# Kernel optimization log

Hardware: AMD Instinct MI355X
Metric: run time of the kernel (lower is better)

Reference implementation:

```python
import jax, jax.numpy as jnp
import numpy as np

N_NUM = 2048      # recurrent neurons (== input_num)
E_NUM = 1638
OUT_NUM = 512     # readout size
TIME_CONST = 0.1  # LIF leak


def setup_inputs() -> dict:
    key = jax.random.key(0)
    k1, k2, k3, k4, k5 = jax.random.split(key, 5)
    B = 4096
    return {
        "i_": jax.random.normal(k1, (B, N_NUM), dtype=jnp.float32),
        "x": jax.random.normal(k2, (B, N_NUM), dtype=jnp.float32),
        "r": jax.random.normal(k3, (N_NUM, N_NUM), dtype=jnp.float32) * (1.0 / np.sqrt(N_NUM)),
        "f": jax.random.normal(k4, (N_NUM, OUT_NUM), dtype=jnp.float32) * (1.0 / np.sqrt(N_NUM)),
        "b": jax.random.normal(k5, (N_NUM,), dtype=jnp.float32) * 0.01,
    }


def reference(i_, x, r, f, b):
    # EI sign vector: ei_mask is a diagonal matrix diag(signs); mm(ei_mask, A) == signs[:, None] * A
    signs = jnp.where(jnp.arange(N_NUM) < E_NUM, 1.0, -1.0).astype(i_.dtype)
    self_mask = 1.0 - jnp.eye(N_NUM, dtype=i_.dtype)  # no_self: zero diagonal

    # LIF state update: x <- (1 - tau) * x + tau * (i_ + b)   (noise_coeff = 0)
    x_new = (1.0 - TIME_CONST) * x + TIME_CONST * (i_ + b)
    u = jax.nn.relu(x_new)

    # Dale's law + self-mask on recurrent weights; Dale on feedforward weights
    r_eff = signs[:, None] * jnp.abs(r * self_mask)   # [N, N]
    f_eff = signs[:, None] * jnp.abs(f)               # [N, OUT]

    f_out = u @ f_eff   # [B, OUT]
    r_out = u @ r_eff   # [B, N]
    return (f_out, r_out, u)
```

## Files before the change

### kernel.cpp

```cpp
#include <hip/hip_runtime.h>
#include <hip/hip_bf16.h>

#define B_NUM 4096
#define N_NUM 2048
#define E_NUM 1638
#define OUT_NUM 512
#define NTOT 2560
#define KDIM 2048
#define NKT 32

typedef unsigned short u16;
typedef __attribute__((ext_vector_type(8))) __bf16 bf16x8;
typedef __attribute__((ext_vector_type(4))) float f32x4;

__device__ __forceinline__ u16 f2bf(float f) {
  union { float f; unsigned u; } v; v.f = f;
  unsigned r = v.u + 0x7fffu + ((v.u >> 16) & 1u);
  return (u16)(r >> 16);
}

__device__ __forceinline__ void gload16(const u16* src, u16* dst) {
  __builtin_amdgcn_global_load_lds((__attribute__((address_space(1))) void*)src,
                                   (__attribute__((address_space(3))) void*)dst,
                                   16, 0, 0);
}

#define BAR() do { asm volatile("" ::: "memory"); \
                   __builtin_amdgcn_s_barrier();  \
                   asm volatile("" ::: "memory"); } while (0)

__global__ __launch_bounds__(256) void prep_u(const float* __restrict__ in_i,
                                              const float* __restrict__ in_x,
                                              const float* __restrict__ bias,
                                              float* __restrict__ u_f32,
                                              u16* __restrict__ u_bf16) {
  const int t = blockIdx.x * 256 + threadIdx.x;
  const int e = t * 4;
  const float4 iv = *(const float4*)(in_i + e);
  const float4 xv = *(const float4*)(in_x + e);
  const float4 bv = *(const float4*)(bias + (e & (N_NUM - 1)));
  float4 u;
  u.x = fmaxf(0.f, 0.9f * xv.x + 0.1f * (iv.x + bv.x));
  u.y = fmaxf(0.f, 0.9f * xv.y + 0.1f * (iv.y + bv.y));
  u.z = fmaxf(0.f, 0.9f * xv.z + 0.1f * (iv.z + bv.z));
  u.w = fmaxf(0.f, 0.9f * xv.w + 0.1f * (iv.w + bv.w));
  *(float4*)(u_f32 + e) = u;
  ushort4 ub;
  ub.x = f2bf(u.x); ub.y = f2bf(u.y); ub.z = f2bf(u.z); ub.w = f2bf(u.w);
  *(ushort4*)(u_bf16 + e) = ub;
}

__global__ __launch_bounds__(256) void prep_w(const float* __restrict__ r,
                                              const float* __restrict__ f,
                                              u16* __restrict__ wt) {
  __shared__ u16 ldsT[64][72];
  const int k0 = blockIdx.y * 64;
  const int n0 = blockIdx.x * 64;
  const int tid = threadIdx.x;
  const int rloc = tid >> 4;
  const int c4 = (tid & 15) * 4;
#pragma unroll
  for (int rr = 0; rr < 4; ++rr) {
    const int kl = rr * 16 + rloc;
    const int k = k0 + kl;
    const float sign = (k < E_NUM) ? 1.f : -1.f;
    float4 v;
    if (n0 < N_NUM) v = *(const float4*)(r + k * N_NUM + n0 + c4);
    else            v = *(const float4*)(f + k * OUT_NUM + (n0 - N_NUM) + c4);
    float vals[4] = {v.x, v.y, v.z, v.w};
#pragma unroll
    for (int j = 0; j < 4; ++j) {
      float val = sign * fabsf(vals[j]);
      if (n0 < N_NUM && (n0 + c4 + j) == k) val = 0.f;
      ldsT[c4 + j][kl] = f2bf(val);
    }
  }
  __syncthreads();
  const int nl = tid >> 2;
  const int kc = (tid & 3) * 16;
  u16* dst = wt + (n0 + nl) * KDIM + k0 + kc;
  *(uint4*)(dst) = *(const uint4*)&ldsT[nl][kc];
  *(uint4*)(dst + 8) = *(const uint4*)&ldsT[nl][kc + 8];
}

__global__ __launch_bounds__(256, 2) void gemm4(const u16* __restrict__ U,
                                                const u16* __restrict__ Wt,
                                                float* __restrict__ out) {
  __shared__ u16 lds[2][2][128 * 64];
  const int t = threadIdx.x;
  const int w = t >> 6, lane = t & 63;
  const int lr = lane & 15, lg = lane >> 4;
  const int wm = w >> 1, wn = w & 1;
  const int row0 = blockIdx.y * 128;
  const int col0 = blockIdx.x * 128;

  const int srow = t >> 3;
  const int koff = 8 * ((t & 7) ^ (srow & 7));
  const u16* aS = U  + (row0 + srow) * KDIM + koff;
  const u16* bS = Wt + (col0 + srow) * KDIM + koff;
  const int stBase = w * 512;

  const int arow = wm * 64 + lr;
  const int brow = wn * 64 + lr;
  const int xs = (lr & 7) << 4;
  const int ca0 = ((lg * 16) ^ xs) >> 1;
  const int ca1 = ((64 + lg * 16) ^ xs) >> 1;

  f32x4 acc[4][4] = {};

#define STAGE_A(c, kt) { const int k0_ = (kt) * 64;                         \
  _Pragma("unroll") for (int i_ = 0; i_ < 4; ++i_)                          \
    gload16(aS + i_ * 32 * KDIM + k0_, &lds[c][0][i_ * 2048 + stBase]); }
#define STAGE_B(c, kt) { const int k0_ = (kt) * 64;                         \
  _Pragma("unroll") for (int i_ = 0; i_ < 4; ++i_)                          \
    gload16(bS + i_ * 32 * KDIM + k0_, &lds[c][1][i_ * 2048 + stBase]); }

  STAGE_B(0, 0);
  STAGE_A(0, 0);
  STAGE_B(1, 1);
  asm volatile("s_waitcnt vmcnt(4)" ::: "memory");
  __builtin_amdgcn_sched_barrier(0);
  BAR();

  for (int T = 0; T < NKT; ++T) {
    const int c = T & 1;
    const u16* lA = lds[c][0];
    const u16* lB = lds[c][1];
    bf16x8 bf[4][2], af[2][2];
#pragma unroll
    for (int ni = 0; ni < 4; ++ni) {
      bf[ni][0] = *(const bf16x8*)&lB[(brow + ni * 16) * 64 + ca0];
      bf[ni][1] = *(const bf16x8*)&lB[(brow + ni * 16) * 64 + ca1];
    }
#pragma unroll
    for (int mi = 0; mi < 2; ++mi) {
      af[mi][0] = *(const bf16x8*)&lA[(arow + mi * 16) * 64 + ca0];
      af[mi][1] = *(const bf16x8*)&lA[(arow + mi * 16) * 64 + ca1];
    }
    { const int tn = (T + 1 < NKT) ? T + 1 : NKT - 1;
      STAGE_A(c ^ 1, tn); }
    BAR();
    __builtin_amdgcn_s_setprio(1);
#pragma unroll
    for (int mi = 0; mi < 2; ++mi)
#pragma unroll
      for (int ni = 0; ni < 4; ++ni) {
        acc[mi][ni] = __builtin_amdgcn_mfma_f32_16x16x32_bf16(af[mi][0], bf[ni][0], acc[mi][ni], 0, 0, 0);
        acc[mi][ni] = __builtin_amdgcn_mfma_f32_16x16x32_bf16(af[mi][1], bf[ni][1], acc[mi][ni], 0, 0, 0);
      }
    __builtin_amdgcn_s_setprio(0);
    BAR();
#pragma unroll
    for (int mi = 0; mi < 2; ++mi) {
      af[mi][0] = *(const bf16x8*)&lA[(arow + 32 + mi * 16) * 64 + ca0];
      af[mi][1] = *(const bf16x8*)&lA[(arow + 32 + mi * 16) * 64 + ca1];
    }
    { const int tn = (T + 2 < NKT) ? T + 2 : NKT - 1;
      STAGE_B(c, tn); }
    BAR();
    __builtin_amdgcn_s_setprio(1);
#pragma unroll
    for (int mi = 0; mi < 2; ++mi)
#pragma unroll
      for (int ni = 0; ni < 4; ++ni) {
        acc[2 + mi][ni] = __builtin_amdgcn_mfma_f32_16x16x32_bf16(af[mi][0], bf[ni][0], acc[2 + mi][ni], 0, 0, 0);
        acc[2 + mi][ni] = __builtin_amdgcn_mfma_f32_16x16x32_bf16(af[mi][1], bf[ni][1], acc[2 + mi][ni], 0, 0, 0);
      }
    __builtin_amdgcn_s_setprio(0);
    asm volatile("s_waitcnt vmcnt(4)" ::: "memory");
    __builtin_amdgcn_sched_barrier(0);
    BAR();
  }
  asm volatile("s_waitcnt vmcnt(0)" ::: "memory");

  const int orow = row0 + wm * 64 + lg * 4;
  const int ocol = col0 + wn * 64 + lr;
  if (col0 < N_NUM) {
    float* ro = out + B_NUM * OUT_NUM;
#pragma unroll
    for (int mi = 0; mi < 4; ++mi)
#pragma unroll
      for (int ni = 0; ni < 4; ++ni)
#pragma unroll
        for (int q = 0; q < 4; ++q)
          ro[(orow + mi * 16 + q) * N_NUM + ocol + ni * 16] = acc[mi][ni][q];
  } else {
#pragma unroll
    for (int mi = 0; mi < 4; ++mi)
#pragma unroll
      for (int ni = 0; ni < 4; ++ni)
#pragma unroll
        for (int q = 0; q < 4; ++q)
          out[(orow + mi * 16 + q) * OUT_NUM + (ocol - N_NUM) + ni * 16] = acc[mi][ni][q];
  }
#undef STAGE_A
#undef STAGE_B
}

extern "C" void kernel_launch(void* const* d_in, const int* in_sizes, int n_in,
                              void* d_out, int out_size, void* d_ws, size_t ws_size,
                              hipStream_t stream) {
  const float* i_ = (const float*)d_in[0];
  const float* x  = (const float*)d_in[1];
  const float* r  = (const float*)d_in[2];
  const float* f  = (const float*)d_in[3];
  const float* b  = (const float*)d_in[4];
  float* out = (float*)d_out;

  u16* U  = (u16*)d_ws;
  u16* Wt = (u16*)((char*)d_ws + (size_t)B_NUM * KDIM * 2);

  float* u_region = out + (size_t)B_NUM * OUT_NUM + (size_t)B_NUM * N_NUM;

  prep_u<<<(B_NUM * N_NUM / 4) / 256, 256, 0, stream>>>(i_, x, b, u_region, U);
  prep_w<<<dim3(NTOT / 64, N_NUM / 64), 256, 0, stream>>>(r, f, Wt);
  gemm4<<<dim3(NTOT / 128, B_NUM / 128), 256, 0, stream>>>(U, Wt, out);
}
```

Before: 198.7 us.

## Load GEMM A fragments directly into registers and stage only B in LDS

The GEMM no longer stages the activation (A) tile in shared memory. Each wave loads its A fragments straight from global memory into registers, double-buffered one K-tile ahead, while only the weight (B) tile goes through LDS via global_load_lds. The main loop is restructured into two half-steps per K-tile with fewer barriers, and shared memory use is halved. The aim is to cut LDS traffic and synchronisation. In exchange, A is read redundantly from global/L2 by both column waves, global load latency is hidden by only one tile of prefetch, and register pressure is higher.

```diff
diff --git a/kernel.cpp b/kernel.cpp
--- a/kernel.cpp
+++ b/kernel.cpp
@@ -83,10 +83,10 @@
   *(uint4*)(dst + 8) = *(const uint4*)&ldsT[nl][kc + 8];
 }
 
-__global__ __launch_bounds__(256, 2) void gemm4(const u16* __restrict__ U,
-                                                const u16* __restrict__ Wt,
-                                                float* __restrict__ out) {
-  __shared__ u16 lds[2][2][128 * 64];
+__global__ __launch_bounds__(256, 2) void gemm4d(const u16* __restrict__ U,
+                                                 const u16* __restrict__ Wt,
+                                                 float* __restrict__ out) {
+  __shared__ u16 lds[2][128 * 64];
   const int t = threadIdx.x;
   const int w = t >> 6, lane = t & 63;
   const int lr = lane & 15, lg = lane >> 4;
@@ -96,80 +96,63 @@
 
   const int srow = t >> 3;
   const int koff = 8 * ((t & 7) ^ (srow & 7));
-  const u16* aS = U  + (row0 + srow) * KDIM + koff;
   const u16* bS = Wt + (col0 + srow) * KDIM + koff;
   const int stBase = w * 512;
 
-  const int arow = wm * 64 + lr;
   const int brow = wn * 64 + lr;
   const int xs = (lr & 7) << 4;
   const int ca0 = ((lg * 16) ^ xs) >> 1;
   const int ca1 = ((64 + lg * 16) ^ xs) >> 1;
 
+  const u16* aF = U + (size_t)(row0 + wm * 64 + lr) * KDIM + lg * 8;
+
   f32x4 acc[4][4] = {};
-
-#define STAGE_A(c, kt) { const int k0_ = (kt) * 64;                         \
+  bf16x8 afA[4][2], afB[4][2], bf[4][2];
+
+#define STB(c, kt) { const u16* g_ = bS + (kt) * 64;                        \
   _Pragma("unroll") for (int i_ = 0; i_ < 4; ++i_)                          \
-    gload16(aS + i_ * 32 * KDIM + k0_, &lds[c][0][i_ * 2048 + stBase]); }
-#define STAGE_B(c, kt) { const int k0_ = (kt) * 64;                         \
-  _Pragma("unroll") for (int i_ = 0; i_ < 4; ++i_)                          \
-    gload16(bS + i_ * 32 * KDIM + k0_, &lds[c][1][i_ * 2048 + stBase]); }
-
-  STAGE_B(0, 0);
-  STAGE_A(0, 0);
-  STAGE_B(1, 1);
+    gload16(g_ + i_ * 32 * KDIM, &lds[c][i_ * 2048 + stBase]); }
+#define LOAD_A(dst, kt) { _Pragma("unroll") for (int mi = 0; mi < 4; ++mi) {\
+    dst[mi][0] = *(const bf16x8*)(aF + mi * 16 * KDIM + (kt) * 64);         \
+    dst[mi][1] = *(const bf16x8*)(aF + mi * 16 * KDIM + (kt) * 64 + 32); } }
+#define RD_B(c) { _Pragma("unroll") for (int ni = 0; ni < 4; ++ni) {        \
+    bf[ni][0] = *(const bf16x8*)&lds[c][(brow + ni * 16) * 64 + ca0];       \
+    bf[ni][1] = *(const bf16x8*)&lds[c][(brow + ni * 16) * 64 + ca1]; } }
+#define MFMA_KS(AF, ks) { _Pragma("unroll") for (int mi = 0; mi < 4; ++mi)  \
+    _Pragma("unroll") for (int ni = 0; ni < 4; ++ni)                        \
+      acc[mi][ni] = __builtin_amdgcn_mfma_f32_16x16x32_bf16(                \
+          AF[mi][ks], bf[ni][ks], acc[mi][ni], 0, 0, 0); }
+
+#define KTILE(c, AFC, AFN, Tn, Tb) {                                        \
+    RD_B(c);                                                                \
+    LOAD_A(AFN, Tn);                                                        \
+    __builtin_amdgcn_s_setprio(1);                                          \
+    MFMA_KS(AFC, 0);                                                        \
+    __builtin_amdgcn_sched_barrier(0);                                      \
+    asm volatile("s_waitcnt lgkmcnt(0)" ::: "memory");                      \
+    __builtin_amdgcn_sched_barrier(0);                                      \
+    __builtin_amdgcn_s_barrier();                                           \
+    STB(c, Tb);                                                             \
+    MFMA_KS(AFC, 1);                                                        \
+    __builtin_amdgcn_s_setprio(0);                                          \
+    asm volatile("s_waitcnt vmcnt(4)" ::: "memory");                        \
+    __builtin_amdgcn_sched_barrier(0);                                      \
+    __builtin_amdgcn_s_barrier(); }
+
+  STB(0, 0);
+  LOAD_A(afA, 0);
+  STB(1, 1);
   asm volatile("s_waitcnt vmcnt(4)" ::: "memory");
   __builtin_amdgcn_sched_barrier(0);
   BAR();
 
-  for (int T = 0; T < NKT; ++T) {
-    const int c = T & 1;
-    const u16* lA = lds[c][0];
-    const u16* lB = lds[c][1];
-    bf16x8 bf[4][2], af[2][2];
-#pragma unroll
-    for (int ni = 0; ni < 4; ++ni) {
-      bf[ni][0] = *(const bf16x8*)&lB[(brow + ni * 16) * 64 + ca0];
-      bf[ni][1] = *(const bf16x8*)&lB[(brow + ni * 16) * 64 + ca1];
-    }
-#pragma unroll
-    for (int mi = 0; mi < 2; ++mi) {
-      af[mi][0] = *(const bf16x8*)&lA[(arow + mi * 16) * 64 + ca0];
-      af[mi][1] = *(const bf16x8*)&lA[(arow + mi * 16) * 64 + ca1];
-    }
-    { const int tn = (T + 1 < NKT) ? T + 1 : NKT - 1;
-      STAGE_A(c ^ 1, tn); }
-    BAR();
-    __builtin_amdgcn_s_setprio(1);
-#pragma unroll
-    for (int mi = 0; mi < 2; ++mi)
-#pragma unroll
-      for (int ni = 0; ni < 4; ++ni) {
-        acc[mi][ni] = __builtin_amdgcn_mfma_f32_16x16x32_bf16(af[mi][0], bf[ni][0], acc[mi][ni], 0, 0, 0);
-        acc[mi][ni] = __builtin_amdgcn_mfma_f32_16x16x32_bf16(af[mi][1], bf[ni][1], acc[mi][ni], 0, 0, 0);
-      }
-    __builtin_amdgcn_s_setprio(0);
-    BAR();
-#pragma unroll
-    for (int mi = 0; mi < 2; ++mi) {
-      af[mi][0] = *(const bf16x8*)&lA[(arow + 32 + mi * 16) * 64 + ca0];
-      af[mi][1] = *(const bf16x8*)&lA[(arow + 32 + mi * 16) * 64 + ca1];
-    }
-    { const int tn = (T + 2 < NKT) ? T + 2 : NKT - 1;
-      STAGE_B(c, tn); }
-    BAR();
-    __builtin_amdgcn_s_setprio(1);
-#pragma unroll
-    for (int mi = 0; mi < 2; ++mi)
-#pragma unroll
-      for (int ni = 0; ni < 4; ++ni) {
-        acc[2 + mi][ni] = __builtin_amdgcn_mfma_f32_16x16x32_bf16(af[mi][0], bf[ni][0], acc[2 + mi][ni], 0, 0, 0);
-        acc[2 + mi][ni] = __builtin_amdgcn_mfma_f32_16x16x32_bf16(af[mi][1], bf[ni][1], acc[2 + mi][ni], 0, 0, 0);
-      }
-    __builtin_amdgcn_s_setprio(0);
-    asm volatile("s_waitcnt vmcnt(4)" ::: "memory");
-    __builtin_amdgcn_sched_barrier(0);
-    BAR();
+  for (int it = 0; it < NKT / 2; ++it) {
+    const int T = 2 * it;
+    const int t1 = (T + 1 < NKT) ? T + 1 : NKT - 1;
+    const int t2 = (T + 2 < NKT) ? T + 2 : NKT - 1;
+    const int t3 = (T + 3 < NKT) ? T + 3 : NKT - 1;
+    KTILE(0, afA, afB, t1, t2);
+    KTILE(1, afB, afA, t2, t3);
   }
   asm volatile("s_waitcnt vmcnt(0)" ::: "memory");
 
@@ -193,8 +176,11 @@
         for (int q = 0; q < 4; ++q)
           out[(orow + mi * 16 + q) * OUT_NUM + (ocol - N_NUM) + ni * 16] = acc[mi][ni][q];
   }
-#undef STAGE_A
-#undef STAGE_B
+#undef STB
+#undef LOAD_A
+#undef RD_B
+#undef MFMA_KS
+#undef KTILE
 }
 
 extern "C" void kernel_launch(void* const* d_in, const int* in_sizes, int n_in,
@@ -214,5 +200,5 @@
 
   prep_u<<<(B_NUM * N_NUM / 4) / 256, 256, 0, stream>>>(i_, x, b, u_region, U);
   prep_w<<<dim3(NTOT / 64, N_NUM / 64), 256, 0, stream>>>(r, f, Wt);
-  gemm4<<<dim3(NTOT / 128, B_NUM / 128), 256, 0, stream>>>(U, Wt, out);
-}
+  gemm4d<<<dim3(NTOT / 128, B_NUM / 128), 256, 0, stream>>>(U, Wt, out);
+}
```

Result: slower. 259.4 us (+30.5%).
